# Performance work log

Measured on AMD Instinct MI355X. Metric: run time of the kernel, lower is better.

## Reference

```python
import jax, jax.numpy as jnp
import numpy as np

P, B, D, H, O = 512, 8, 256, 75, 128  # passage_len, batch, input_size, attn hidden, GRU hidden


def setup_inputs() -> dict:
    key = jax.random.key(0)
    ks = jax.random.split(key, 10)

    def w(k, shape, fan_in):
        return jax.random.normal(k, shape, jnp.float32) * (1.0 / np.sqrt(fan_in))

    return {
        "v": jax.random.normal(ks[0], (P, B, D), jnp.float32),
        "Wvp1": w(ks[1], (H, D), D),          # nn.Linear(input_size, hidden, bias=False)
        "Wvp2": w(ks[2], (H, D), D),
        "vw": w(ks[3], (H,), H),               # nn.Linear(hidden, 1, bias=False)
        "Wg": w(ks[4], (2 * D, 2 * D), 2 * D),  # Gate linear, no bias
        "w_ih_f": w(ks[5], (3 * O, 2 * D), 2 * D),
        "w_hh_f": w(ks[6], (3 * O, O), O),
        "b_ih_f": jnp.zeros((3 * O,), jnp.float32),
        "b_hh_f": jnp.zeros((3 * O,), jnp.float32),
        "w_ih_b": w(ks[7], (3 * O, 2 * D), 2 * D),
        "w_hh_b": w(ks[8], (3 * O, O), O),
        "b_ih_b": jnp.zeros((3 * O,), jnp.float32),
        "b_hh_b": jnp.zeros((3 * O,), jnp.float32),
    }


def _gru(x, w_ih, w_hh, b_ih, b_hh):
    # x: (T, B, in) -> hidden states (T, B, O); PyTorch GRU gate order (r, z, n)
    hdim = w_hh.shape[1]
    xp = x @ w_ih.T + b_ih  # precompute input projections: (T, B, 3O)

    def step(h, xp_t):
        gh = h @ w_hh.T + b_hh
        i_r, i_z, i_n = jnp.split(xp_t, 3, axis=-1)
        h_r, h_z, h_n = jnp.split(gh, 3, axis=-1)
        r = jax.nn.sigmoid(i_r + h_r)
        z = jax.nn.sigmoid(i_z + h_z)
        n = jnp.tanh(i_n + r * h_n)
        h_new = (1.0 - z) * n + z * h
        return h_new, h_new

    h0 = jnp.zeros((x.shape[1], hdim), x.dtype)
    _, hs = jax.lax.scan(step, h0, xp)
    return hs


def reference(v, Wvp1, Wvp2, vw, Wg,
              w_ih_f, w_hh_f, b_ih_f, b_hh_f,
              w_ih_b, w_hh_b, b_ih_b, b_hh_b):
    # dropout is inference no-op (and in the torch code its result is discarded anyway)
    Wv1 = v @ Wvp1.T  # (P, B, H) -- broadcast over key axis (dim 1 after expand)
    Wv2 = v @ Wvp2.T  # (P, B, H) -- broadcast over query axis
    # s[i, j, b, h] = tanh(Wv2[i] + Wv1[j]); softmax over i (keys)
    s = jnp.tanh(Wv2[:, None] + Wv1[None, :])          # (P, P, B, H)
    scores = jnp.einsum('ijbh,h->ijb', s, vw)          # (P, P, B)
    a = jax.nn.softmax(scores, axis=0)
    c = jnp.einsum('ijb,ibd->jbd', a, v)               # attended context (P, B, D)
    g = jnp.concatenate([v, c], axis=2)                # (P, B, 2D)
    g = jax.nn.sigmoid(g @ Wg.T) * g                   # Gate
    hf = _gru(g, w_ih_f, w_hh_f, b_ih_f, b_hh_f)
    hb = _gru(g[::-1], w_ih_b, w_hh_b, b_ih_b, b_hh_b)[::-1]
    return jnp.concatenate([hf, hb], axis=2)           # (P, B, 2O)
```

## Files before the change

### kernel.cpp

```cpp
#include <hip/hip_runtime.h>

#define TP 512
#define TB 8
#define TD 256
#define TH 75
#define THP 80
#define TO 128

typedef _Float16 half_t;
typedef _Float16 half2v __attribute__((ext_vector_type(2)));
typedef _Float16 half4v __attribute__((ext_vector_type(4)));
typedef _Float16 half8v __attribute__((ext_vector_type(8)));
typedef float    float4v __attribute__((ext_vector_type(4)));

__device__ __forceinline__ float fast_rcp(float x) { return __builtin_amdgcn_rcpf(x); }
__device__ __forceinline__ float fast_tanh(float x) {
    return 1.0f - 2.0f * fast_rcp(1.0f + __expf(2.0f * x));
}
__device__ __forceinline__ float fast_sigmoid(float x) {
    return fast_rcp(1.0f + __expf(-x));
}
__device__ __forceinline__ float fdot2h(half2v a, half2v b, float c) {
#if __has_builtin(__builtin_amdgcn_fdot2)
    return __builtin_amdgcn_fdot2(a, b, c, false);
#else
    return c + (float)a[0] * (float)b[0] + (float)a[1] * (float)b[1];
#endif
}
#define EXT2(v, j) __builtin_shufflevector((v), (v), 2*(j), 2*(j)+1)
__device__ __forceinline__ void dot3_h8(half8v wr, half8v wz, half8v wn, half8v h,
                                        float& ar, float& az, float& an) {
    half2v h0 = EXT2(h, 0), h1 = EXT2(h, 1), h2 = EXT2(h, 2), h3 = EXT2(h, 3);
    ar = fdot2h(EXT2(wr, 0), h0, ar);
    az = fdot2h(EXT2(wz, 0), h0, az);
    an = fdot2h(EXT2(wn, 0), h0, an);
    ar = fdot2h(EXT2(wr, 1), h1, ar);
    az = fdot2h(EXT2(wz, 1), h1, az);
    an = fdot2h(EXT2(wn, 1), h1, an);
    ar = fdot2h(EXT2(wr, 2), h2, ar);
    az = fdot2h(EXT2(wz, 2), h2, az);
    an = fdot2h(EXT2(wn, 2), h2, an);
    ar = fdot2h(EXT2(wr, 3), h3, ar);
    az = fdot2h(EXT2(wz, 3), h3, az);
    an = fdot2h(EXT2(wn, 3), h3, an);
}
__device__ __forceinline__ float pair_sum_dpp(float v) {
    int i1 = __builtin_amdgcn_update_dpp(0, __builtin_bit_cast(int, v), 0xB1, 0xF, 0xF, true);
    return v + __builtin_bit_cast(float, i1);
}

__global__ __launch_bounds__(256) void prep_kernel(
    const float* __restrict__ v,
    const float* __restrict__ Wvp1, const float* __restrict__ Wvp2,
    const float* __restrict__ Wg,   const float* __restrict__ wihf,
    const float* __restrict__ wihb, const float* __restrict__ bihf,
    const float* __restrict__ bihb, const float* __restrict__ whhf,
    const float* __restrict__ whhb,
    float* __restrict__ bihC,
    half_t* __restrict__ v16, half_t* __restrict__ g16,
    half_t* __restrict__ Wg16B, half_t* __restrict__ Wih16B,
    half_t* __restrict__ whh16, half_t* __restrict__ WT16B)
{
    int idx = blockIdx.x * 256 + threadIdx.x;
    if (idx < 1048576) {
        half_t val = (half_t)v[idx];
        v16[idx] = val;
        int row = idx >> 8, d = idx & 255;
        g16[row * 512 + d] = val;
        return;
    }
    idx -= 1048576;
    if (idx < 768) { bihC[idx] = (idx < 384) ? bihf[idx] : bihb[idx - 384]; return; }
    idx -= 768;
    if (idx < 262144) {
        int j = idx & 7, lane = (idx >> 3) & 63, kt = (idx >> 9) & 15, nt = idx >> 13;
        int o = nt * 16 + (lane & 15);
        int k = kt * 32 + ((lane >> 4) << 3) + j;
        Wg16B[idx] = (half_t)Wg[o * 512 + k];
        return;
    }
    idx -= 262144;
    if (idx < 393216) {
        int j = idx & 7, lane = (idx >> 3) & 63, kt = (idx >> 9) & 15, nt = idx >> 13;
        int o = nt * 16 + (lane & 15);
        int k = kt * 32 + ((lane >> 4) << 3) + j;
        Wih16B[idx] = (half_t)((o < 384) ? wihf[o * 512 + k] : wihb[(o - 384) * 512 + k]);
        return;
    }
    idx -= 393216;
    if (idx < 98304) {
        int d = idx / 49152, i = idx - d * 49152;
        whh16[idx] = (half_t)(d ? whhb[i] : whhf[i]);
        return;
    }
    idx -= 98304;
    if (idx < 40960) {
        int j = idx & 7, lane = (idx >> 3) & 63, kt = (idx >> 9) & 7, nt = idx >> 12;
        int o = nt * 16 + (lane & 15);
        int k = kt * 32 + ((lane >> 4) << 3) + j;
        float vv = 0.0f;
        if (o < 75)       vv = Wvp1[o * 256 + k];
        else if (o < 150) vv = Wvp2[(o - 75) * 256 + k];
        WT16B[idx] = (half_t)vv;
    }
}

__global__ __launch_bounds__(256) void vtrans_kernel(
    const float* __restrict__ v, half_t* __restrict__ vT16)
{
    __shared__ half_t lt[64 * 66];
    int t = threadIdx.x;
    int b  = blockIdx.x >> 5;
    int pt = (blockIdx.x >> 2) & 7;
    int dt = blockIdx.x & 3;

    {
        int pl = t >> 2, dseg = (t & 3) * 16;
        const float4* src = (const float4*)(v + (((pt * 64 + pl) * 8 + b) << 8) + dt * 64 + dseg);
        float4 f0 = src[0], f1 = src[1], f2 = src[2], f3 = src[3];
        half_t hv[16] = {
            (half_t)f0.x,(half_t)f0.y,(half_t)f0.z,(half_t)f0.w,
            (half_t)f1.x,(half_t)f1.y,(half_t)f1.z,(half_t)f1.w,
            (half_t)f2.x,(half_t)f2.y,(half_t)f2.z,(half_t)f2.w,
            (half_t)f3.x,(half_t)f3.y,(half_t)f3.z,(half_t)f3.w };
#pragma unroll
        for (int u = 0; u < 16; ++u) lt[(dseg + u) * 66 + pl] = hv[u];
    }
    __syncthreads();
    {
        int dl = t >> 2, pseg = (t & 3) * 16;
        half8v h0 = *(const half8v*)(lt + dl * 66 + pseg);
        half8v h1 = *(const half8v*)(lt + dl * 66 + pseg + 8);
        half8v* dst = (half8v*)(vT16 + ((b * 256 + dt * 64 + dl) << 9) + pt * 64 + pseg);
        dst[0] = h0; dst[1] = h1;
    }
}

__global__ __launch_bounds__(256) void wv12_kernel(
    const half_t* __restrict__ v16, const half_t* __restrict__ WT16B,
    float* __restrict__ Wv1, float* __restrict__ Wv2T)
{
    int tid = threadIdx.x;
    int lane = tid & 63, w = tid >> 6;
    int l15 = lane & 15, quad = lane >> 4;
    int r0 = blockIdx.x * 64 + w * 16;

    float4v acc[10];
#pragma unroll
    for (int nt = 0; nt < 10; ++nt) acc[nt] = (float4v){0.f, 0.f, 0.f, 0.f};

#pragma unroll
    for (int kt = 0; kt < 8; ++kt) {
        half8v a = *(const half8v*)(v16 + (r0 + l15) * 256 + kt * 32 + quad * 8);
#pragma unroll
        for (int nt = 0; nt < 10; ++nt) {
            half8v b = *(const half8v*)(WT16B + ((nt * 8 + kt) * 64 + lane) * 8);
            acc[nt] = __builtin_amdgcn_mfma_f32_16x16x32_f16(a, b, acc[nt], 0, 0, 0);
        }
    }
#pragma unroll
    for (int nt = 0; nt < 10; ++nt) {
        int col = nt * 16 + l15;
#pragma unroll
        for (int r = 0; r < 4; ++r) {
            int row = r0 + quad * 4 + r;
            int p = row >> 3, b = row & 7;
            int ob = (b * TP + p) * THP;
            float val2 = 2.0f * acc[nt][r];
            if (col < 75)       Wv1[ob + col] = val2;
            else if (col < 80)  { Wv1[ob + col] = 0.0f;
                                  Wv2T[(b * THP + col - 75) * TP + p] = val2; }
            else if (col < 150) Wv2T[(b * THP + col - 75) * TP + p] = val2;
            else if (col < 155) Wv2T[(b * THP + col - 75) * TP + p] = 0.0f;
        }
    }
}

__global__ __launch_bounds__(256) void score_kernel(
    const float* __restrict__ Wv1, const float* __restrict__ Wv2T,
    const float* __restrict__ vw, half_t* __restrict__ a16)
{
    int tid = threadIdx.x;
    int b  = blockIdx.x >> 7;
    int j0 = (blockIdx.x & 127) * 4;
    __shared__ float wv1j[4 * THP];
    __shared__ float vws[THP];
    __shared__ float sc[4 * TP];

    if (tid < THP) vws[tid] = (tid < TH) ? vw[tid] : 0.0f;
    for (int e = tid; e < 4 * THP; e += 256) {
        int jj = e / THP, k = e - jj * THP;
        wv1j[e] = Wv1[(b * TP + j0 + jj) * THP + k];
    }
    __syncthreads();

    float Csum = 0.0f;
    {
        const float4* c4 = (const float4*)vws;
        for (int kk = 0; kk < 20; ++kk) { float4 c = c4[kk]; Csum += c.x + c.y + c.z + c.w; }
    }

    int i0 = tid, i1 = tid + 256;
    float acc0[4] = {0.f,0.f,0.f,0.f}, acc1[4] = {0.f,0.f,0.f,0.f};
    const float* wvt = Wv2T + b * THP * TP;
#pragma unroll
    for (int kt = 0; kt < 5; ++kt) {
        float r0v[16], r1v[16];
#pragma unroll
        for (int u = 0; u < 16; ++u) {
            const float* colp = wvt + (kt * 16 + u) * TP;
            r0v[u] = colp[i0];
            r1v[u] = colp[i1];
        }
        const float* cp = vws + kt * 16;
#pragma unroll
        for (int jj = 0; jj < 4; ++jj) {
            const float* w1 = wv1j + jj * THP + kt * 16;
            float s0 = 0.f, s1 = 0.f;
#pragma unroll
            for (int u = 0; u < 16; ++u) {
                float cu = cp[u], wu = w1[u];
                s0 += cu * fast_rcp(1.0f + __expf(r0v[u] + wu));
                s1 += cu * fast_rcp(1.0f + __expf(r1v[u] + wu));
            }
            acc0[jj] += s0; acc1[jj] += s1;
        }
    }
#pragma unroll
    for (int jj = 0; jj < 4; ++jj) {
        sc[jj * TP + i0] = Csum - 2.0f * acc0[jj];
        sc[jj * TP + i1] = Csum - 2.0f * acc1[jj];
    }
    __syncthreads();

    {
        int jj = tid >> 6, l = tid & 63;
        float m = -1e30f;
#pragma unroll
        for (int q = 0; q < 8; ++q) m = fmaxf(m, sc[jj * TP + l + q * 64]);
#pragma unroll
        for (int s = 32; s > 0; s >>= 1) m = fmaxf(m, __shfl_xor(m, s));
        float e[8];
        float sum = 0.0f;
#pragma unroll
        for (int q = 0; q < 8; ++q) { e[q] = __expf(sc[jj * TP + l + q * 64] - m); sum += e[q]; }
#pragma unroll
        for (int s = 32; s > 0; s >>= 1) sum += __shfl_xor(sum, s);
        float inv = fast_rcp(sum);
        half_t* arow = a16 + (b * TP + j0 + jj) * TP;
#pragma unroll
        for (int q = 0; q < 8; ++q) arow[l + q * 64] = (half_t)(e[q] * inv);
    }
}

__global__ __launch_bounds__(256) void context_kernel(
    const half_t* __restrict__ a16, const half_t* __restrict__ vT16,
    half_t* __restrict__ g16)
{
    int tid = threadIdx.x;
    int lane = tid & 63, w = tid >> 6;
    int l15 = lane & 15, quad = lane >> 4;
    int b  = blockIdx.x >> 5;
    int mt = blockIdx.x & 31;

    const half_t* arow = a16 + (b * TP + mt * 16 + l15) * TP;
    const half_t* vbase = vT16 + ((b * 256) << 9);

    float4v acc[4];
#pragma unroll
    for (int nti = 0; nti < 4; ++nti) acc[nti] = (float4v){0.f, 0.f, 0.f, 0.f};

#pragma unroll 4
    for (int kt = 0; kt < 16; ++kt) {
        half8v a = *(const half8v*)(arow + kt * 32 + quad * 8);
#pragma unroll
        for (int nti = 0; nti < 4; ++nti) {
            int d = (w * 4 + nti) * 16 + l15;
            half8v bb = *(const half8v*)(vbase + (d << 9) + kt * 32 + quad * 8);
            acc[nti] = __builtin_amdgcn_mfma_f32_16x16x32_f16(a, bb, acc[nti], 0, 0, 0);
        }
    }
#pragma unroll
    for (int nti = 0; nti < 4; ++nti) {
        int d = (w * 4 + nti) * 16 + l15;
#pragma unroll
        for (int r = 0; r < 4; ++r) {
            int j = mt * 16 + quad * 4 + r;
            g16[(j * TB + b) * 512 + 256 + d] = (half_t)acc[nti][r];
        }
    }
}

__global__ __launch_bounds__(256, 1) void gatexp_kernel(
    const half_t* __restrict__ g16, const half_t* __restrict__ Wg16B,
    const half_t* __restrict__ Wih16B, const float* __restrict__ bihC,
    float* __restrict__ xpf, float* __restrict__ xpb)
{
    __shared__ half_t gA[32 * 520];
    int tid = threadIdx.x;
    int r0 = blockIdx.x * 32;
    int lane = tid & 63, w = tid >> 6;
    int l15 = lane & 15, quad = lane >> 4;

    for (int e = tid; e < 2048; e += 256) {
        int row = e >> 6, c8 = e & 63;
        *(half8v*)(gA + row * 520 + c8 * 8) =
            *(const half8v*)(g16 + (r0 + row) * 512 + c8 * 8);
    }
    __syncthreads();

    float4v acc[2][8];
#pragma unroll
    for (int mi = 0; mi < 2; ++mi)
#pragma unroll
        for (int nti = 0; nti < 8; ++nti) acc[mi][nti] = (float4v){0.f, 0.f, 0.f, 0.f};

    for (int kt = 0; kt < 16; ++kt) {
        half8v a0 = *(const half8v*)(gA + l15 * 520 + kt * 32 + quad * 8);
        half8v a1 = *(const half8v*)(gA + (16 + l15) * 520 + kt * 32 + quad * 8);
#pragma unroll
        for (int nti = 0; nti < 8; ++nti) {
            half8v bb = *(const half8v*)(Wg16B + (((w * 8 + nti) * 16 + kt) * 64 + lane) * 8);
            acc[0][nti] = __builtin_amdgcn_mfma_f32_16x16x32_f16(a0, bb, acc[0][nti], 0, 0, 0);
            acc[1][nti] = __builtin_amdgcn_mfma_f32_16x16x32_f16(a1, bb, acc[1][nti], 0, 0, 0);
        }
    }
#pragma unroll
    for (int mi = 0; mi < 2; ++mi)
#pragma unroll
        for (int nti = 0; nti < 8; ++nti) {
            int colg = (w * 8 + nti) * 16 + l15;
#pragma unroll
            for (int r = 0; r < 4; ++r) {
                float gv = (float)gA[(mi * 16 + quad * 4 + r) * 520 + colg];
                acc[mi][nti][r] = fast_sigmoid(acc[mi][nti][r]) * gv;
            }
        }
    __syncthreads();
#pragma unroll
    for (int mi = 0; mi < 2; ++mi)
#pragma unroll
        for (int nti = 0; nti < 8; ++nti) {
            int colg = (w * 8 + nti) * 16 + l15;
#pragma unroll
            for (int r = 0; r < 4; ++r)
                gA[(mi * 16 + quad * 4 + r) * 520 + colg] = (half_t)acc[mi][nti][r];
        }
    __syncthreads();

    float4v c2[2][12];
#pragma unroll
    for (int mi = 0; mi < 2; ++mi)
#pragma unroll
        for (int nt2 = 0; nt2 < 12; ++nt2) {
            float bv = bihC[(w * 12 + nt2) * 16 + l15];
            c2[mi][nt2] = (float4v){bv, bv, bv, bv};
        }

    for (int kt = 0; kt < 16; ++kt) {
        half8v a0 = *(const half8v*)(gA + l15 * 520 + kt * 32 + quad * 8);
        half8v a1 = *(const half8v*)(gA + (16 + l15) * 520 + kt * 32 + quad * 8);
#pragma unroll
        for (int nt2 = 0; nt2 < 12; ++nt2) {
            half8v bb = *(const half8v*)(Wih16B + (((w * 12 + nt2) * 16 + kt) * 64 + lane) * 8);
            c2[0][nt2] = __builtin_amdgcn_mfma_f32_16x16x32_f16(a0, bb, c2[0][nt2], 0, 0, 0);
            c2[1][nt2] = __builtin_amdgcn_mfma_f32_16x16x32_f16(a1, bb, c2[1][nt2], 0, 0, 0);
        }
    }
#pragma unroll
    for (int mi = 0; mi < 2; ++mi)
#pragma unroll
        for (int nt2 = 0; nt2 < 12; ++nt2) {
            int col = (w * 12 + nt2) * 16 + l15;
            float* dst = (col < 384) ? (xpf + col) : (xpb + col - 384);
#pragma unroll
            for (int r = 0; r < 4; ++r)
                dst[(r0 + mi * 16 + quad * 4 + r) * 384] = c2[mi][nt2][r];
        }
}

__global__ __launch_bounds__(256, 1) void gru_kernel(
    const float* __restrict__ xpf, const float* __restrict__ xpb,
    const half_t* __restrict__ whh16,
    const float* __restrict__ bhhf, const float* __restrict__ bhhb,
    float* __restrict__ out)
{
    int tid = threadIdx.x;
    int dir = blockIdx.x >> 3;
    int b   = blockIdx.x & 7;
    const float* xp  = dir ? xpb  : xpf;
    const float* bhh = dir ? bhhb : bhhf;
    const half_t* wbase = whh16 + dir * 3 * TO * TO;

    __shared__ __align__(16) half_t hb[2][TO];

    int o = tid >> 1, hf = tid & 1;

    half8v wr[8], wz[8], wn[8];
    {
        const half8v* pr = (const half8v*)(wbase + (o)          * TO + hf * 64);
        const half8v* pz = (const half8v*)(wbase + (TO + o)     * TO + hf * 64);
        const half8v* pn = (const half8v*)(wbase + (2 * TO + o) * TO + hf * 64);
#pragma unroll
        for (int kk = 0; kk < 8; ++kk) { wr[kk] = pr[kk]; wz[kk] = pz[kk]; wn[kk] = pn[kk]; }
    }
#pragma unroll
    for (int kk = 0; kk < 8; ++kk) {
        asm volatile("" : "+v"(wr[kk]), "+v"(wz[kk]), "+v"(wn[kk]));
    }

    float br = 0.f, bz = 0.f, bn = 0.f, h = 0.f;
    if (hf == 0) {
        br = bhh[o]; bz = bhh[TO + o]; bn = bhh[2 * TO + o];
    }
    if (tid < TO) hb[0][tid] = (half_t)0.0f;
    __syncthreads();

    float xrv[8], xzv[8], xnv[8];
    float nxr[8], nxz[8], nxn[8];
    float hist[8];

    if (hf == 0) {
#pragma unroll
        for (int u = 0; u < 8; ++u) {
            int tn = dir ? (TP - 1 - u) : u;
            const float* xpt = xp + (tn * TB + b) * 384;
            nxr[u] = xpt[o]; nxz[u] = xpt[TO + o]; nxn[u] = xpt[2 * TO + o];
        }
    }

    for (int S = 0; S < TP; S += 8) {
        if (hf == 0) {
#pragma unroll
            for (int u = 0; u < 8; ++u) { xrv[u] = nxr[u]; xzv[u] = nxz[u]; xnv[u] = nxn[u]; }
            if (S + 8 < TP) {
#pragma unroll
                for (int u = 0; u < 8; ++u) {
                    int s = S + 8 + u;
                    int tn = dir ? (TP - 1 - s) : s;
                    const float* xpt = xp + (tn * TB + b) * 384;
                    nxr[u] = xpt[o]; nxz[u] = xpt[TO + o]; nxn[u] = xpt[2 * TO + o];
                }
            }
        }
#pragma unroll
        for (int u = 0; u < 8; ++u) {
            int s = S + u;
            int cur = s & 1;
            const half8v* h8 = (const half8v*)(&hb[cur][hf * 64]);
            half8v hv0 = h8[0], hv1 = h8[1], hv2 = h8[2], hv3 = h8[3];
            half8v hv4 = h8[4], hv5 = h8[5], hv6 = h8[6], hv7 = h8[7];

            float ar = 0.f, az = 0.f, an = 0.f;
            dot3_h8(wr[0], wz[0], wn[0], hv0, ar, az, an);
            dot3_h8(wr[1], wz[1], wn[1], hv1, ar, az, an);
            dot3_h8(wr[2], wz[2], wn[2], hv2, ar, az, an);
            dot3_h8(wr[3], wz[3], wn[3], hv3, ar, az, an);
            dot3_h8(wr[4], wz[4], wn[4], hv4, ar, az, an);
            dot3_h8(wr[5], wz[5], wn[5], hv5, ar, az, an);
            dot3_h8(wr[6], wz[6], wn[6], hv6, ar, az, an);
            dot3_h8(wr[7], wz[7], wn[7], hv7, ar, az, an);

            ar = pair_sum_dpp(ar);
            az = pair_sum_dpp(az);
            an = pair_sum_dpp(an);
            if (hf == 0) {
                float r = fast_sigmoid(xrv[u] + ar + br);
                float z = fast_sigmoid(xzv[u] + az + bz);
                float n = fast_tanh(xnv[u] + r * (an + bn));
                h = (1.0f - z) * n + z * h;
                hb[cur ^ 1][o] = (half_t)h;
                hist[u] = h;
            }
            asm volatile("s_waitcnt lgkmcnt(0)" ::: "memory");
            __builtin_amdgcn_s_barrier();
            __builtin_amdgcn_sched_barrier(0);
        }
        if (hf == 0) {
#pragma unroll
            for (int u = 0; u < 8; ++u) {
                int s = S + u;
                int t = dir ? (TP - 1 - s) : s;
                out[(t * TB + b) * 256 + dir * TO + o] = hist[u];
            }
        }
    }
}

extern "C" void kernel_launch(void* const* d_in, const int* in_sizes, int n_in,
                              void* d_out, int out_size, void* d_ws, size_t ws_size,
                              hipStream_t stream) {
    const float* v    = (const float*)d_in[0];
    const float* Wvp1 = (const float*)d_in[1];
    const float* Wvp2 = (const float*)d_in[2];
    const float* vw   = (const float*)d_in[3];
    const float* Wg   = (const float*)d_in[4];
    const float* wihf = (const float*)d_in[5];
    const float* whhf = (const float*)d_in[6];
    const float* bihf = (const float*)d_in[7];
    const float* bhhf = (const float*)d_in[8];
    const float* wihb = (const float*)d_in[9];
    const float* whhb = (const float*)d_in[10];
    const float* bihb = (const float*)d_in[11];
    const float* bhhb = (const float*)d_in[12];

    float* ws   = (float*)d_ws;
    float* bihC = ws;
    float* Wv1  = bihC + 768;
    float* Wv2T = Wv1 + 327680;
    float* xpf  = Wv2T + 327680;
    float* xpb  = xpf + 1572864;
    half_t* g16    = (half_t*)(xpb + 1572864);
    half_t* Wg16B  = g16 + 2097152;
    half_t* Wih16B = Wg16B + 262144;
    half_t* whh16  = Wih16B + 393216;
    half_t* v16    = whh16 + 98304;
    half_t* WT16B  = v16 + 1048576;
    half_t* vT16   = WT16B + 40960;
    half_t* a16    = vT16 + 1048576;
    float* out  = (float*)d_out;

    prep_kernel<<<7203, 256, 0, stream>>>(v, Wvp1, Wvp2, Wg, wihf, wihb, bihf, bihb,
                                          whhf, whhb, bihC, v16, g16,
                                          Wg16B, Wih16B, whh16, WT16B);
    vtrans_kernel<<<256, 256, 0, stream>>>(v, vT16);
    wv12_kernel<<<64, 256, 0, stream>>>(v16, WT16B, Wv1, Wv2T);
    score_kernel<<<1024, 256, 0, stream>>>(Wv1, Wv2T, vw, a16);
    context_kernel<<<256, 256, 0, stream>>>(a16, vT16, g16);
    gatexp_kernel<<<128, 256, 0, stream>>>(g16, Wg16B, Wih16B, bihC, xpf, xpb);
    gru_kernel<<<16, 256, 0, stream>>>(xpf, xpb, whh16, bhhf, bhhb, out);
}
```

Measured before the change: 456.8 us.

## Split GRU recurrent dot products across four lanes per hidden unit with 512 threads

The GRU recurrence kernel now launches 512 threads per block, giving each hidden unit four lanes that each handle a 32-element slice of the recurrent matvec instead of two lanes handling 64 elements. A two-stage DPP quad reduction replaces the pair reduction. Input-projection loads and biases are spread across the quad lanes and folded into the accumulator initial values, so the per-step critical path is shorter. The cost is more waves synchronising at each step's block barrier, and the hand-written waitcnt/s_barrier sequence is replaced by __syncthreads.

```diff
diff --git a/kernel.cpp b/kernel.cpp
--- a/kernel.cpp
+++ b/kernel.cpp
@@ -44,9 +44,11 @@
     az = fdot2h(EXT2(wz, 3), h3, az);
     an = fdot2h(EXT2(wn, 3), h3, an);
 }
-__device__ __forceinline__ float pair_sum_dpp(float v) {
-    int i1 = __builtin_amdgcn_update_dpp(0, __builtin_bit_cast(int, v), 0xB1, 0xF, 0xF, true);
-    return v + __builtin_bit_cast(float, i1);
+__device__ __forceinline__ float quad_sum_dpp(float v) {
+    int a = __builtin_amdgcn_update_dpp(0, __builtin_bit_cast(int, v), 0xB1, 0xF, 0xF, true);
+    v = v + __builtin_bit_cast(float, a);
+    int c = __builtin_amdgcn_update_dpp(0, __builtin_bit_cast(int, v), 0x4E, 0xF, 0xF, true);
+    return v + __builtin_bit_cast(float, c);
 }
 
 __global__ __launch_bounds__(256) void prep_kernel(
@@ -379,7 +381,7 @@
         }
 }
 
-__global__ __launch_bounds__(256, 1) void gru_kernel(
+__global__ __launch_bounds__(512, 2) void gru_kernel(
     const float* __restrict__ xpf, const float* __restrict__ xpb,
     const half_t* __restrict__ whh16,
     const float* __restrict__ bhhf, const float* __restrict__ bhhb,
@@ -394,52 +396,81 @@
 
     __shared__ __align__(16) half_t hb[2][TO];
 
-    int o = tid >> 1, hf = tid & 1;
-
-    half8v wr[8], wz[8], wn[8];
+    int o = tid >> 2, q = tid & 3;
+
+    half8v wr[4], wz[4], wn[4];
     {
-        const half8v* pr = (const half8v*)(wbase + (o)          * TO + hf * 64);
-        const half8v* pz = (const half8v*)(wbase + (TO + o)     * TO + hf * 64);
-        const half8v* pn = (const half8v*)(wbase + (2 * TO + o) * TO + hf * 64);
-#pragma unroll
-        for (int kk = 0; kk < 8; ++kk) { wr[kk] = pr[kk]; wz[kk] = pz[kk]; wn[kk] = pn[kk]; }
-    }
-#pragma unroll
-    for (int kk = 0; kk < 8; ++kk) {
-        asm volatile("" : "+v"(wr[kk]), "+v"(wz[kk]), "+v"(wn[kk]));
+        const half8v* pr = (const half8v*)(wbase + (o)          * TO + q * 32);
+        const half8v* pz = (const half8v*)(wbase + (TO + o)     * TO + q * 32);
+        const half8v* pn = (const half8v*)(wbase + (2 * TO + o) * TO + q * 32);
+#pragma unroll
+        for (int kk = 0; kk < 4; ++kk) { wr[kk] = pr[kk]; wz[kk] = pz[kk]; wn[kk] = pn[kk]; }
     }
 
     float br = 0.f, bz = 0.f, bn = 0.f, h = 0.f;
-    if (hf == 0) {
-        br = bhh[o]; bz = bhh[TO + o]; bn = bhh[2 * TO + o];
-    }
+    if (q == 1) br = bhh[o];
+    if (q == 2) bz = bhh[TO + o];
+    if (q == 3) bn = bhh[2 * TO + o];
+
     if (tid < TO) hb[0][tid] = (half_t)0.0f;
     __syncthreads();
 
-    float xrv[8], xzv[8], xnv[8];
-    float nxr[8], nxz[8], nxn[8];
-    float hist[8];
-
-    if (hf == 0) {
+    float xrv[8] = {}, xzv[8] = {}, xnv[8] = {};
+    float nxr[8] = {}, nxz[8] = {}, nxn[8] = {};
+    float hist[8] = {};
+
+    if (q == 1) {
 #pragma unroll
         for (int u = 0; u < 8; ++u) {
             int tn = dir ? (TP - 1 - u) : u;
-            const float* xpt = xp + (tn * TB + b) * 384;
-            nxr[u] = xpt[o]; nxz[u] = xpt[TO + o]; nxn[u] = xpt[2 * TO + o];
+            nxr[u] = xp[(tn * TB + b) * 384 + o];
+        }
+    } else if (q == 2) {
+#pragma unroll
+        for (int u = 0; u < 8; ++u) {
+            int tn = dir ? (TP - 1 - u) : u;
+            nxz[u] = xp[(tn * TB + b) * 384 + TO + o];
+        }
+    } else if (q == 3) {
+#pragma unroll
+        for (int u = 0; u < 8; ++u) {
+            int tn = dir ? (TP - 1 - u) : u;
+            nxn[u] = xp[(tn * TB + b) * 384 + 2 * TO + o];
         }
     }
 
     for (int S = 0; S < TP; S += 8) {
-        if (hf == 0) {
-#pragma unroll
-            for (int u = 0; u < 8; ++u) { xrv[u] = nxr[u]; xzv[u] = nxz[u]; xnv[u] = nxn[u]; }
+        if (q == 1) {
+#pragma unroll
+            for (int u = 0; u < 8; ++u) xrv[u] = nxr[u] + br;
             if (S + 8 < TP) {
 #pragma unroll
                 for (int u = 0; u < 8; ++u) {
                     int s = S + 8 + u;
                     int tn = dir ? (TP - 1 - s) : s;
-                    const float* xpt = xp + (tn * TB + b) * 384;
-                    nxr[u] = xpt[o]; nxz[u] = xpt[TO + o]; nxn[u] = xpt[2 * TO + o];
+                    nxr[u] = xp[(tn * TB + b) * 384 + o];
+                }
+            }
+        } else if (q == 2) {
+#pragma unroll
+            for (int u = 0; u < 8; ++u) xzv[u] = nxz[u] + bz;
+            if (S + 8 < TP) {
+#pragma unroll
+                for (int u = 0; u < 8; ++u) {
+                    int s = S + 8 + u;
+                    int tn = dir ? (TP - 1 - s) : s;
+                    nxz[u] = xp[(tn * TB + b) * 384 + TO + o];
+                }
+            }
+        } else if (q == 3) {
+#pragma unroll
+            for (int u = 0; u < 8; ++u) xnv[u] = nxn[u];
+            if (S + 8 < TP) {
+#pragma unroll
+                for (int u = 0; u < 8; ++u) {
+                    int s = S + 8 + u;
+                    int tn = dir ? (TP - 1 - s) : s;
+                    nxn[u] = xp[(tn * TB + b) * 384 + 2 * TO + o];
                 }
             }
         }
@@ -447,36 +478,31 @@
         for (int u = 0; u < 8; ++u) {
             int s = S + u;
             int cur = s & 1;
-            const half8v* h8 = (const half8v*)(&hb[cur][hf * 64]);
+            const half8v* h8 = (const half8v*)(&hb[cur][q * 32]);
             half8v hv0 = h8[0], hv1 = h8[1], hv2 = h8[2], hv3 = h8[3];
-            half8v hv4 = h8[4], hv5 = h8[5], hv6 = h8[6], hv7 = h8[7];
-
-            float ar = 0.f, az = 0.f, an = 0.f;
+
+            float ar = (q == 1) ? xrv[u] : 0.f;
+            float az = (q == 2) ? xzv[u] : 0.f;
+            float an = (q == 3) ? bn     : 0.f;
             dot3_h8(wr[0], wz[0], wn[0], hv0, ar, az, an);
             dot3_h8(wr[1], wz[1], wn[1], hv1, ar, az, an);
             dot3_h8(wr[2], wz[2], wn[2], hv2, ar, az, an);
             dot3_h8(wr[3], wz[3], wn[3], hv3, ar, az, an);
-            dot3_h8(wr[4], wz[4], wn[4], hv4, ar, az, an);
-            dot3_h8(wr[5], wz[5], wn[5], hv5, ar, az, an);
-            dot3_h8(wr[6], wz[6], wn[6], hv6, ar, az, an);
-            dot3_h8(wr[7], wz[7], wn[7], hv7, ar, az, an);
-
-            ar = pair_sum_dpp(ar);
-            az = pair_sum_dpp(az);
-            an = pair_sum_dpp(an);
-            if (hf == 0) {
-                float r = fast_sigmoid(xrv[u] + ar + br);
-                float z = fast_sigmoid(xzv[u] + az + bz);
-                float n = fast_tanh(xnv[u] + r * (an + bn));
+
+            ar = quad_sum_dpp(ar);
+            az = quad_sum_dpp(az);
+            an = quad_sum_dpp(an);
+            if (q == 3) {
+                float r = fast_sigmoid(ar);
+                float z = fast_sigmoid(az);
+                float n = fast_tanh(xnv[u] + r * an);
                 h = (1.0f - z) * n + z * h;
                 hb[cur ^ 1][o] = (half_t)h;
                 hist[u] = h;
             }
-            asm volatile("s_waitcnt lgkmcnt(0)" ::: "memory");
-            __builtin_amdgcn_s_barrier();
-            __builtin_amdgcn_sched_barrier(0);
-        }
-        if (hf == 0) {
+            __syncthreads();
+        }
+        if (q == 3) {
 #pragma unroll
             for (int u = 0; u < 8; ++u) {
                 int s = S + u;
@@ -528,5 +554,5 @@
     score_kernel<<<1024, 256, 0, stream>>>(Wv1, Wv2T, vw, a16);
     context_kernel<<<256, 256, 0, stream>>>(a16, vT16, g16);
     gatexp_kernel<<<128, 256, 0, stream>>>(g16, Wg16B, Wih16B, bihC, xpf, xpb);
-    gru_kernel<<<16, 256, 0, stream>>>(xpf, xpb, whh16, bhhf, bhhb, out);
-}
+    gru_kernel<<<16, 512, 0, stream>>>(xpf, xpb, whh16, bhhf, bhhb, out);
+}
```

Result: slower. 539.7 us (+18.1%).
